# Kernel tuning notes

Hardware: AMD Instinct MI355X
Metric: run time of the kernel (lower is better)

Reference implementation:

```python
import jax, jax.numpy as jnp
import numpy as np
import math

EMBED_DIM = 768
NUM_HEADS = 12
HEAD_DIM = EMBED_DIM // NUM_HEADS
R = 16
LORA_ALPHA = 16
SCALING = LORA_ALPHA / math.sqrt(R)  # 4.0
U = 1.0  # ramp_up_steps=0 -> u()=1.0


def lora_linear(x, W, b, A):
    # base F.linear + SingLoRA delta: delta_W = A @ A.T (symmetric)
    base = x @ W.T + b
    delta_W = A @ A.T  # [D, D]
    return base + (x @ delta_W.T) * (U * SCALING)


def setup_inputs() -> dict:
    key = jax.random.key(0)
    ks = jax.random.split(key, 16)
    B, S, D = 2, 2048, EMBED_DIM
    inv = 1.0 / math.sqrt(D)
    d = {
        'query': jax.random.normal(ks[0], (B, S, D), jnp.float32),
        'key': jax.random.normal(ks[1], (B, S, D), jnp.float32),
        'value': jax.random.normal(ks[2], (B, S, D), jnp.float32),
        'Wq': jax.random.normal(ks[3], (D, D), jnp.float32) * inv,
        'bq': jax.random.normal(ks[4], (D,), jnp.float32) * 0.01,
        'Aq': jax.random.normal(ks[5], (D, R), jnp.float32) * 0.01,
        'Wk': jax.random.normal(ks[6], (D, D), jnp.float32) * inv,
        'bk': jax.random.normal(ks[7], (D,), jnp.float32) * 0.01,
        'Ak': jax.random.normal(ks[8], (D, R), jnp.float32) * 0.01,
        'Wv': jax.random.normal(ks[9], (D, D), jnp.float32) * inv,
        'bv': jax.random.normal(ks[10], (D,), jnp.float32) * 0.01,
        'Av': jax.random.normal(ks[11], (D, R), jnp.float32) * 0.01,
        'Wo': jax.random.normal(ks[12], (D, D), jnp.float32) * inv,
        'bo': jax.random.normal(ks[13], (D,), jnp.float32) * 0.01,
    }
    return d


def reference(query, key, value, Wq, bq, Aq, Wk, bk, Ak, Wv, bv, Av, Wo, bo):
    B, S, D = query.shape
    H, hd = NUM_HEADS, HEAD_DIM
    q = lora_linear(query, Wq, bq, Aq)
    k = lora_linear(key, Wk, bk, Ak)
    v = lora_linear(value, Wv, bv, Av)
    # [B, S, D] -> [B, H, S, hd]
    q = q.reshape(B, S, H, hd).transpose(0, 2, 1, 3)
    k = k.reshape(B, S, H, hd).transpose(0, 2, 1, 3)
    v = v.reshape(B, S, H, hd).transpose(0, 2, 1, 3)
    scores = jnp.einsum('bhqd,bhkd->bhqk', q, k) / math.sqrt(hd)
    attn = jax.nn.softmax(scores, axis=-1)
    out = jnp.einsum('bhqk,bhkd->bhqd', attn, v)  # [B, H, S, hd]
    out = out.transpose(0, 2, 1, 3).reshape(B, S, D)
    out = out @ Wo.T + bo
    return out
```

## Files before the change

### kernel.cpp

```cpp
#include <hip/hip_runtime.h>
#include <math.h>
#include <stdint.h>

#define D 768
#define S 2048
#define B_ 2
#define NROWS 4096
#define H 12
#define HD 64
#define R_ 16

typedef _Float16 half_t;
typedef _Float16 half8 __attribute__((ext_vector_type(8)));
typedef _Float16 half4 __attribute__((ext_vector_type(4)));
typedef float floatx4 __attribute__((ext_vector_type(4)));

#define MFMA32(a, b, c) __builtin_amdgcn_mfma_f32_16x16x32_f16(a, b, c, 0, 0, 0)
#define EXP2F(x) __builtin_amdgcn_exp2f(x)

#define SWAIT(N) __builtin_amdgcn_s_waitcnt(0x0F70 | (N))
#define SBAR() __builtin_amdgcn_s_barrier()
#define SETPRIO(N) __builtin_amdgcn_s_setprio(N)

__device__ __forceinline__ void gl_lds16(const void* gp, half_t* lp) {
  __builtin_amdgcn_global_load_lds(
      (const __attribute__((address_space(1))) void*)(gp),
      (__attribute__((address_space(3))) void*)(lp), 16, 0, 0);
}


__global__ __launch_bounds__(256) void prep_kernel(
    const float* __restrict__ q, const float* __restrict__ k,
    const float* __restrict__ v, half_t* __restrict__ xq,
    half_t* __restrict__ xk, half_t* __restrict__ xv,
    const float* __restrict__ Wq, const float* __restrict__ Aq,
    const float* __restrict__ Wk, const float* __restrict__ Ak,
    const float* __restrict__ Wv, const float* __restrict__ Av,
    const float* __restrict__ Wo, half_t* __restrict__ Mq,
    half_t* __restrict__ Mk, half_t* __restrict__ Mv,
    half_t* __restrict__ Mo) {
  __shared__ float4 As[3072];
  const int bid = blockIdx.x;
  const int tid = threadIdx.x;

  if (bid < 2304) {
    const int y = bid / 768;
    const float* x = (y == 0) ? q : (y == 1) ? k : v;
    half_t* o = (y == 0) ? xq : (y == 1) ? xk : xv;
    const int base = (bid - y * 768) * 4096;
#pragma unroll
    for (int c = 0; c < 4; ++c) {
      int i = base + (tid + 256 * c) * 4;
      float4 vv = *reinterpret_cast<const float4*>(x + i);
      half_t tmp[4] = {(half_t)vv.x, (half_t)vv.y, (half_t)vv.z, (half_t)vv.w};
      *reinterpret_cast<uint64_t*>(o + i) = *reinterpret_cast<uint64_t*>(tmp);
    }
  } else if (bid < 2448) {
    const int base = (bid - 2304) * 4096;
#pragma unroll
    for (int c = 0; c < 4; ++c) {
      int i = base + (tid + 256 * c) * 4;
      float4 vv = *reinterpret_cast<const float4*>(Wo + i);
      half_t tmp[4] = {(half_t)vv.x, (half_t)vv.y, (half_t)vv.z, (half_t)vv.w};
      *reinterpret_cast<uint64_t*>(Mo + i) = *reinterpret_cast<uint64_t*>(tmp);
    }
  } else {
    const int u = bid - 2448;
    const int y = u / 192;
    const int jb = u - y * 192;
    const float* W = (y == 0) ? Wq : (y == 1) ? Wk : Wv;
    const float* A = (y == 0) ? Aq : (y == 1) ? Ak : Av;
    half_t* M = (y == 0) ? Mq : (y == 1) ? Mk : Mv;

#pragma unroll
    for (int c = 0; c < 12; ++c)
      As[tid + 256 * c] =
          *reinterpret_cast<const float4*>(A + (tid + 256 * c) * 4);
    __syncthreads();

    const int j0 = jb * 4;
    float4 aj[4][4];
#pragma unroll
    for (int jj = 0; jj < 4; ++jj)
#pragma unroll
      for (int qq = 0; qq < 4; ++qq) aj[jj][qq] = As[(j0 + jj) * 4 + qq];

#pragma unroll
    for (int c = 0; c < 3; ++c) {
      const int kk = tid + 256 * c;
      float4 ak[4];
#pragma unroll
      for (int qq = 0; qq < 4; ++qq) ak[qq] = As[kk * 4 + qq];
#pragma unroll
      for (int jj = 0; jj < 4; ++jj) {
        float s = 0.f;
#pragma unroll
        for (int qq = 0; qq < 4; ++qq)
          s += ak[qq].x * aj[jj][qq].x + ak[qq].y * aj[jj][qq].y +
               ak[qq].z * aj[jj][qq].z + ak[qq].w * aj[jj][qq].w;
        const int idx = (j0 + jj) * D + kk;
        M[idx] = (half_t)(W[idx] + 4.0f * s);
      }
    }
  }
}

__global__ __launch_bounds__(256) void gemm_qkv_kernel(
    const half_t* __restrict__ x0, const half_t* __restrict__ x1,
    const half_t* __restrict__ x2, const half_t* __restrict__ m0,
    const half_t* __restrict__ m1, const half_t* __restrict__ m2,
    const float* __restrict__ b0, const float* __restrict__ b1,
    const float* __restrict__ b2, half_t* __restrict__ o0,
    half_t* __restrict__ o1, half_t* __restrict__ o2) {
  constexpr int AG = 8;
  constexpr int G = 14;
  constexpr int PB = G * 512;
  __shared__ __align__(16) half_t smem[3 * PB];

  int lin = blockIdx.x + 8 * (blockIdx.y + 32 * blockIdx.z);
  lin = (lin & 7) * 96 + (lin >> 3);
  const int z = lin / 256;
  const int rem = lin - z * 256;
  const int by = rem >> 3;
  const int bx = rem & 7;

  const half_t* X = (z == 0) ? x0 : (z == 1) ? x1 : x2;
  const half_t* M = (z == 0) ? m0 : (z == 1) ? m1 : m2;
  const float* bias = (z == 0) ? b0 : (z == 1) ? b1 : b2;
  half_t* Out = (z == 0) ? o0 : (z == 1) ? o1 : o2;

  const int tid = threadIdx.x;
  const int lane = tid & 63;
  const int wv = tid >> 6;
  const int lr = lane & 15;
  const int lq = lane >> 4;
  const int row0 = by * 128;
  const int j0 = bx * 96;
  const int wr = wv >> 1;
  const int wc = wv & 1;
  const int heavy = __builtin_amdgcn_readfirstlane(wv < 2 ? 1 : 0);

  floatx4 acc[4][3] = {};

#define GSTAGE(soff, k0)                                                      \
  do {                                                                        \
    _Pragma("unroll") for (int gi = 0; gi < 4; ++gi) {                        \
      int g = wv + gi * 4;                                                    \
      if (g < AG) {                                                           \
        gl_lds16(X + (size_t)(row0 + g * 16 + lr) * D + (k0) + lq * 8,        \
                 smem + (soff) + g * 512);                                    \
      } else if (g < G) {                                                     \
        gl_lds16(M + (size_t)(j0 + (g - AG) * 16 + lr) * D + (k0) + lq * 8,   \
                 smem + (soff) + g * 512);                                    \
      }                                                                       \
    }                                                                         \
  } while (0)

#define QWAIT()                                                               \
  do {                                                                        \
    if (heavy) SWAIT(4); else SWAIT(3);                                       \
  } while (0)

  GSTAGE(0, 0);
  GSTAGE(PB, 32);
  QWAIT();
  SBAR();

  int co = 0, so = 2 * PB;
  for (int it = 0; it < D / 32; ++it) {
    if (it + 2 < D / 32) GSTAGE(so, (it + 2) * 32);
    const half_t* Ab = smem + co;
    const half_t* Bb = Ab + AG * 512;
    half8 af[4], bf[3];
#pragma unroll
    for (int t = 0; t < 4; ++t)
      af[t] = *reinterpret_cast<const half8*>(
          &Ab[((wr * 4 + t) * 64 + lane) * 8]);
#pragma unroll
    for (int u = 0; u < 3; ++u)
      bf[u] = *reinterpret_cast<const half8*>(
          &Bb[((wc * 3 + u) * 64 + lane) * 8]);
#pragma unroll
    for (int t = 0; t < 4; ++t)
#pragma unroll
      for (int u = 0; u < 3; ++u) acc[t][u] = MFMA32(af[t], bf[u], acc[t][u]);
    if (it + 2 < D / 32) QWAIT(); else SWAIT(0);
    SBAR();
    co += PB; if (co == 3 * PB) co = 0;
    so += PB; if (so == 3 * PB) so = 0;
  }
#undef GSTAGE
#undef QWAIT

  float bv[3];
#pragma unroll
  for (int u = 0; u < 3; ++u) bv[u] = bias[j0 + (wc * 3 + u) * 16 + lr];

  if (z == 2) {
    const int bb = row0 >> 11;
    const int kb0 = (row0 & 2047) >> 6;
#pragma unroll
    for (int t = 0; t < 4; ++t) {
#pragma unroll
      for (int u = 0; u < 3; ++u) {
        int gc = j0 + (wc * 3 + u) * 16 + lr;
        int hh = gc >> 6;
        int ud = (gc & 63) >> 4;
        half4 hv;
#pragma unroll
        for (int r = 0; r < 4; ++r) hv[r] = (half_t)(acc[t][u][r] + bv[u]);
        size_t addr = ((size_t)(bb * H + hh) * HD) * S +
                      (size_t)(kb0 + wr) * 4096 +
                      (ud * 2 + ((t >> 1) & 1)) * 512 + lane * 8 + (t & 1) * 4;
        *reinterpret_cast<half4*>(&Out[addr]) = hv;
      }
    }
    return;
  }

#pragma unroll
  for (int t = 0; t < 4; ++t) {
#pragma unroll
    for (int u = 0; u < 3; ++u) {
#pragma unroll
      for (int r = 0; r < 4; ++r) {
        int gr = row0 + (wr * 4 + t) * 16 + lq * 4 + r;
        int gc = j0 + (wc * 3 + u) * 16 + lr;
        Out[(size_t)gr * D + gc] = (half_t)(acc[t][u][r] + bv[u]);
      }
    }
  }
}

__global__ __launch_bounds__(256) void gemm_o_kernel(
    const half_t* __restrict__ Xh, const half_t* __restrict__ M,
    const float* __restrict__ bias, float* __restrict__ Out) {
  constexpr int AG = 8;
  constexpr int G = 16;
  constexpr int PB = G * 512;
  __shared__ __align__(16) half_t smem[3 * PB];

  int lin = blockIdx.x + 12 * blockIdx.y;
  lin = (lin & 7) * 96 + (lin >> 3);
  const int bx = lin % 12;
  const int byy = lin / 12;

  const int tid = threadIdx.x;
  const int lane = tid & 63;
  const int wv = tid >> 6;
  const int lr = lane & 15;
  const int lq = lane >> 4;
  const int row0 = byy * 64;
  const int j0 = bx * 64;
  const int wr = wv >> 1;
  const int wc = wv & 1;

  floatx4 acc[2][2] = {};

#define GSTAGE(soff, k0)                                                       \
  do {                                                                         \
    _Pragma("unroll") for (int gi = 0; gi < 4; ++gi) {                         \
      int g = wv * 4 + gi;                                                     \
      if (g < AG) {                                                            \
        int t = g >> 1, c = g & 1;                                             \
        gl_lds16(                                                              \
            Xh + (size_t)(row0 + t * 16 + lr) * D + (k0) + c * 32 + lq * 8,    \
            smem + (soff) + g * 512);                                          \
      } else {                                                                 \
        int g2 = g - AG;                                                       \
        int u = g2 >> 1, c = g2 & 1;                                           \
        gl_lds16(                                                              \
            M + (size_t)(j0 + u * 16 + lr) * D + (k0) + c * 32 + lq * 8,       \
            smem + (soff) + AG * 512 + g2 * 512);                              \
      }                                                                        \
    }                                                                          \
  } while (0)

  GSTAGE(0, 0);
  GSTAGE(PB, 64);
  SWAIT(4);
  SBAR();

  int co = 0, so = 2 * PB;
  for (int it = 0; it < D / 64; ++it) {
    if (it + 2 < D / 64) GSTAGE(so, (it + 2) * 64);
    const half_t* Ab = smem + co;
    const half_t* Bb = Ab + AG * 512;
#pragma unroll
    for (int c = 0; c < 2; ++c) {
      half8 af[2], bf[2];
#pragma unroll
      for (int t = 0; t < 2; ++t)
        af[t] = *reinterpret_cast<const half8*>(
            &Ab[(((wr * 2 + t) * 2 + c) * 64 + lane) * 8]);
#pragma unroll
      for (int u = 0; u < 2; ++u)
        bf[u] = *reinterpret_cast<const half8*>(
            &Bb[(((wc * 2 + u) * 2 + c) * 64 + lane) * 8]);
#pragma unroll
      for (int t = 0; t < 2; ++t)
#pragma unroll
        for (int u = 0; u < 2; ++u) acc[t][u] = MFMA32(af[t], bf[u], acc[t][u]);
    }
    if (it + 2 < D / 64) SWAIT(4); else SWAIT(0);
    SBAR();
    co += PB; if (co == 3 * PB) co = 0;
    so += PB; if (so == 3 * PB) so = 0;
  }
#undef GSTAGE

  float bv[2];
#pragma unroll
  for (int u = 0; u < 2; ++u) bv[u] = bias[j0 + (wc * 2 + u) * 16 + lr];
#pragma unroll
  for (int t = 0; t < 2; ++t) {
#pragma unroll
    for (int u = 0; u < 2; ++u) {
#pragma unroll
      for (int r = 0; r < 4; ++r) {
        int gr = row0 + (wr * 2 + t) * 16 + lq * 4 + r;
        int gc = j0 + (wc * 2 + u) * 16 + lr;
        Out[(size_t)gr * D + gc] = acc[t][u][r] + bv[u];
      }
    }
  }
}

__global__ __launch_bounds__(256, 3) void attn_mfma_kernel(
    const half_t* __restrict__ Qh, const half_t* __restrict__ Kh,
    const half_t* __restrict__ Vt2, half_t* __restrict__ Oh) {
  __shared__ __align__(16) half_t smem[24576];
  half_t* Ks = smem;
  half_t* Vs = smem + 12288;

  const int tid = threadIdx.x;
  const int lane = tid & 63;
  const int wv = tid >> 6;
  const int qp = wv >> 1;
  const int half_ = wv & 1;
  const int lr = lane & 15;
  const int lq = lane >> 4;

  int lin = blockIdx.x + 32 * (blockIdx.y + 12 * blockIdx.z);
  lin = (lin & 7) * 96 + (lin >> 3);
  const int q0 = (lin & 31) * 64;
  const int hb = lin >> 5;
  const int h = hb % 12;
  const int b = hb / 12;

  const size_t base = (size_t)b * S * D + h * HD;
  const size_t vtbase = (size_t)(b * H + h) * HD * (size_t)S;

  const half_t qscale = (half_t)0.18033688f;
  half8 qf[2][2];
#pragma unroll
  for (int s = 0; s < 2; ++s) {
    const int qw = q0 + (qp * 2 + s) * 16;
#pragma unroll
    for (int c = 0; c < 2; ++c) {
      half8 qv = *reinterpret_cast<const half8*>(
          &Qh[base + (size_t)(qw + lr) * D + c * 32 + lq * 8]);
#pragma unroll
      for (int j = 0; j < 8; ++j) qv[j] = qv[j] * qscale;
      qf[s][c] = qv;
    }
  }

  half8 ones8;
#pragma unroll
  for (int j = 0; j < 8; ++j) ones8[j] = (half_t)1.0f;

  floatx4 o[2][4] = {};
  floatx4 ol[2] = {};

#define STAGE(soff, kb)                                                        \
  do {                                                                         \
    _Pragma("unroll") for (int gi = 0; gi < 4; ++gi) {                         \
      int g = wv * 4 + gi;                                                     \
      if (g < 8) {                                                             \
        int u = g >> 1, c = g & 1;                                             \
        gl_lds16(                                                              \
            Kh + base + (size_t)((kb) + u * 16 + lr) * D + c * 32 + lq * 8,    \
            Ks + (soff) + g * 512);                                            \
      } else {                                                                 \
        int gv = g - 8;                                                        \
        gl_lds16(Vt2 + vtbase + (size_t)(kb)*64 + gv * 512 + lane * 8,         \
                 Vs + (soff) + gv * 512);                                      \
      }                                                                        \
    }                                                                          \
  } while (0)

  STAGE(0, 0);
  STAGE(4096, 64);
  SWAIT(4);
  SBAR();

  int co = 0, so = 8192;
  for (int it = 0; it < S / 64; ++it) {
    if (it + 2 < S / 64) STAGE(so, (it + 2) * 64);

    half8 pv[2];
#pragma unroll
    for (int ui = 0; ui < 2; ++ui) {
      const int u = half_ * 2 + ui;
      half8 kf0 = *reinterpret_cast<const half8*>(
          &Ks[co + ((u * 2 + 0) * 64 + lane) * 8]);
      half8 kf1 = *reinterpret_cast<const half8*>(
          &Ks[co + ((u * 2 + 1) * 64 + lane) * 8]);
      SETPRIO(1);
      floatx4 st0 = {}, st1 = {};
      st0 = MFMA32(kf0, qf[0][0], st0);
      st0 = MFMA32(kf1, qf[0][1], st0);
      st1 = MFMA32(kf0, qf[1][0], st1);
      st1 = MFMA32(kf1, qf[1][1], st1);
      SETPRIO(0);
#pragma unroll
      for (int j = 0; j < 4; ++j) {
        pv[0][4 * ui + j] = (half_t)EXP2F(st0[j]);
        pv[1][4 * ui + j] = (half_t)EXP2F(st1[j]);
      }
    }
    SETPRIO(1);
#pragma unroll
    for (int ud = 0; ud < 4; ++ud) {
      half8 vf8 = *reinterpret_cast<const half8*>(
          &Vs[co + ((ud * 2 + half_) * 64 + lane) * 8]);
      o[0][ud] = MFMA32(pv[0], vf8, o[0][ud]);
      o[1][ud] = MFMA32(pv[1], vf8, o[1][ud]);
    }
    ol[0] = MFMA32(pv[0], ones8, ol[0]);
    ol[1] = MFMA32(pv[1], ones8, ol[1]);
    SETPRIO(0);

    if (it + 2 < S / 64) SWAIT(4); else SWAIT(0);
    SBAR();
    co += 4096; if (co == 12288) co = 0;
    so += 4096; if (so == 12288) so = 0;
  }
#undef STAGE

  float* red = (float*)smem;
  if (half_ == 1) {
#pragma unroll
    for (int s = 0; s < 2; ++s) {
      const int slot = (qp * 2 + s) * 64 + lane;
#pragma unroll
      for (int comp = 0; comp < 16; ++comp)
        red[comp * 260 + slot] = o[s][comp >> 2][comp & 3];
#pragma unroll
      for (int r = 0; r < 4; ++r) red[(16 + r) * 260 + slot] = ol[s][r];
    }
  }
  __syncthreads();
  if (half_ == 0) {
#pragma unroll
    for (int s = 0; s < 2; ++s) {
      const int slot = (qp * 2 + s) * 64 + lane;
      const int qw = q0 + (qp * 2 + s) * 16;
      float linv[4];
#pragma unroll
      for (int r = 0; r < 4; ++r)
        linv[r] = 1.0f / (ol[s][r] + red[(16 + r) * 260 + slot]);
#pragma unroll
      for (int ud = 0; ud < 4; ++ud) {
#pragma unroll
        for (int r = 0; r < 4; ++r) {
          float ov = o[s][ud][r] + red[(ud * 4 + r) * 260 + slot];
          int row = qw + lq * 4 + r;
          int col = h * HD + ud * 16 + lr;
          Oh[(size_t)(b * S + row) * D + col] = (half_t)(ov * linv[r]);
        }
      }
    }
  }
}

extern "C" void kernel_launch(void* const* d_in, const int* in_sizes, int n_in,
                              void* d_out, int out_size, void* d_ws,
                              size_t ws_size, hipStream_t stream) {
  const float* query = (const float*)d_in[0];
  const float* key   = (const float*)d_in[1];
  const float* value = (const float*)d_in[2];
  const float* Wq = (const float*)d_in[3];
  const float* bq = (const float*)d_in[4];
  const float* Aq = (const float*)d_in[5];
  const float* Wk = (const float*)d_in[6];
  const float* bk = (const float*)d_in[7];
  const float* Ak = (const float*)d_in[8];
  const float* Wv = (const float*)d_in[9];
  const float* bv = (const float*)d_in[10];
  const float* Av = (const float*)d_in[11];
  const float* Wo = (const float*)d_in[12];
  const float* bo = (const float*)d_in[13];
  float* out = (float*)d_out;

  half_t* hw = (half_t*)d_ws;
  const size_t XSZ = (size_t)NROWS * D;
  const size_t MSZ = (size_t)D * D;
  half_t* xq = hw;
  half_t* xk = xq + XSZ;
  half_t* xv = xk + XSZ;
  half_t* qh = xv + XSZ;
  half_t* kh = qh + XSZ;
  half_t* vt = kh + XSZ;
  half_t* ab = vt + XSZ;
  half_t* Mq = ab + XSZ;
  half_t* Mk = Mq + MSZ;
  half_t* Mv = Mk + MSZ;
  half_t* Mo = Mv + MSZ;

  prep_kernel<<<3024, 256, 0, stream>>>(query, key, value, xq, xk, xv, Wq, Aq,
                                        Wk, Ak, Wv, Av, Wo, Mq, Mk, Mv, Mo);

  dim3 gq(D / 96, NROWS / 128, 3);
  gemm_qkv_kernel<<<gq, 256, 0, stream>>>(xq, xk, xv, Mq, Mk, Mv, bq, bk, bv,
                                          qh, kh, vt);

  dim3 ga(S / 64, H, B_);
  attn_mfma_kernel<<<ga, 256, 0, stream>>>(qh, kh, vt, ab);

  dim3 go(D / 64, NROWS / 64, 1);
  gemm_o_kernel<<<go, 256, 0, stream>>>(ab, Mo, bo, out);
}
```

Before: 200.8 us.

## Give each wave private double-buffered LDS slices to remove per-tile block barriers

Each wave now stages only the K and V chunks it consumes into its own private LDS region, double-buffered. This removes the shared triple-buffered staging and the per-iteration block-wide barrier. Synchronization becomes per-wave vmcnt and lgkmcnt waits, and the LDS footprint grows to 64KB, so launch bounds drop from 3 to 2 blocks per SU. The trade-off is lower occupancy and duplicated loads of K across the two waves of each pair in exchange for barrier-free pipelining.

```diff
diff --git a/kernel.cpp b/kernel.cpp
--- a/kernel.cpp
+++ b/kernel.cpp
@@ -19,6 +19,7 @@
 #define EXP2F(x) __builtin_amdgcn_exp2f(x)
 
 #define SWAIT(N) __builtin_amdgcn_s_waitcnt(0x0F70 | (N))
+#define LGWAIT() __builtin_amdgcn_s_waitcnt(0xC07F)
 #define SBAR() __builtin_amdgcn_s_barrier()
 #define SETPRIO(N) __builtin_amdgcn_s_setprio(N)
 
@@ -326,12 +327,10 @@
   }
 }
 
-__global__ __launch_bounds__(256, 3) void attn_mfma_kernel(
+__global__ __launch_bounds__(256, 2) void attn_mfma_kernel(
     const half_t* __restrict__ Qh, const half_t* __restrict__ Kh,
     const half_t* __restrict__ Vt2, half_t* __restrict__ Oh) {
-  __shared__ __align__(16) half_t smem[24576];
-  half_t* Ks = smem;
-  half_t* Vs = smem + 12288;
+  __shared__ __align__(16) half_t smem[32768];
 
   const int tid = threadIdx.x;
   const int lane = tid & 63;
@@ -351,6 +350,8 @@
   const size_t base = (size_t)b * S * D + h * HD;
   const size_t vtbase = (size_t)(b * H + h) * HD * (size_t)S;
 
+  half_t* W0 = smem + wv * 8192;
+
   const half_t qscale = (half_t)0.18033688f;
   half8 qf[2][2];
 #pragma unroll
@@ -373,72 +374,69 @@
   floatx4 o[2][4] = {};
   floatx4 ol[2] = {};
 
-#define STAGE(soff, kb)                                                        \
+#define STAGE(so_, kb)                                                         \
   do {                                                                         \
-    _Pragma("unroll") for (int gi = 0; gi < 4; ++gi) {                         \
-      int g = wv * 4 + gi;                                                     \
-      if (g < 8) {                                                             \
-        int u = g >> 1, c = g & 1;                                             \
-        gl_lds16(                                                              \
-            Kh + base + (size_t)((kb) + u * 16 + lr) * D + c * 32 + lq * 8,    \
-            Ks + (soff) + g * 512);                                            \
-      } else {                                                                 \
-        int gv = g - 8;                                                        \
-        gl_lds16(Vt2 + vtbase + (size_t)(kb)*64 + gv * 512 + lane * 8,         \
-                 Vs + (soff) + gv * 512);                                      \
+    _Pragma("unroll") for (int ui = 0; ui < 2; ++ui)                           \
+      _Pragma("unroll") for (int c = 0; c < 2; ++c)                            \
+        gl_lds16(Kh + base +                                                   \
+                     (size_t)((kb) + (half_ * 2 + ui) * 16 + lr) * D +         \
+                     c * 32 + lq * 8,                                          \
+                 W0 + (so_) + (ui * 2 + c) * 512);                             \
+    _Pragma("unroll") for (int ud = 0; ud < 4; ++ud)                           \
+      gl_lds16(Vt2 + vtbase + (size_t)(kb) * 64 + (ud * 2 + half_) * 512 +     \
+                   lane * 8,                                                   \
+               W0 + (so_) + 2048 + ud * 512);                                  \
+  } while (0)
+
+#define COMP(so_)                                                              \
+  do {                                                                         \
+    half8 pv[2];                                                               \
+    _Pragma("unroll") for (int ui = 0; ui < 2; ++ui) {                         \
+      half8 kf0 = *reinterpret_cast<const half8*>(                             \
+          &W0[(so_) + (ui * 2 + 0) * 512 + lane * 8]);                         \
+      half8 kf1 = *reinterpret_cast<const half8*>(                             \
+          &W0[(so_) + (ui * 2 + 1) * 512 + lane * 8]);                         \
+      SETPRIO(1);                                                              \
+      floatx4 st0 = {}, st1 = {};                                              \
+      st0 = MFMA32(kf0, qf[0][0], st0);                                        \
+      st0 = MFMA32(kf1, qf[0][1], st0);                                        \
+      st1 = MFMA32(kf0, qf[1][0], st1);                                        \
+      st1 = MFMA32(kf1, qf[1][1], st1);                                        \
+      SETPRIO(0);                                                              \
+      _Pragma("unroll") for (int j = 0; j < 4; ++j) {                          \
+        pv[0][4 * ui + j] = (half_t)EXP2F(st0[j]);                             \
+        pv[1][4 * ui + j] = (half_t)EXP2F(st1[j]);                             \
       }                                                                        \
     }                                                                          \
+    SETPRIO(1);                                                                \
+    _Pragma("unroll") for (int ud = 0; ud < 4; ++ud) {                         \
+      half8 vf8 = *reinterpret_cast<const half8*>(                             \
+          &W0[(so_) + 2048 + ud * 512 + lane * 8]);                            \
+      o[0][ud] = MFMA32(pv[0], vf8, o[0][ud]);                                 \
+      o[1][ud] = MFMA32(pv[1], vf8, o[1][ud]);                                 \
+    }                                                                          \
+    ol[0] = MFMA32(pv[0], ones8, ol[0]);                                       \
+    ol[1] = MFMA32(pv[1], ones8, ol[1]);                                       \
+    SETPRIO(0);                                                                \
   } while (0)
 
   STAGE(0, 0);
   STAGE(4096, 64);
-  SWAIT(4);
-  SBAR();
-
-  int co = 0, so = 8192;
-  for (int it = 0; it < S / 64; ++it) {
-    if (it + 2 < S / 64) STAGE(so, (it + 2) * 64);
-
-    half8 pv[2];
-#pragma unroll
-    for (int ui = 0; ui < 2; ++ui) {
-      const int u = half_ * 2 + ui;
-      half8 kf0 = *reinterpret_cast<const half8*>(
-          &Ks[co + ((u * 2 + 0) * 64 + lane) * 8]);
-      half8 kf1 = *reinterpret_cast<const half8*>(
-          &Ks[co + ((u * 2 + 1) * 64 + lane) * 8]);
-      SETPRIO(1);
-      floatx4 st0 = {}, st1 = {};
-      st0 = MFMA32(kf0, qf[0][0], st0);
-      st0 = MFMA32(kf1, qf[0][1], st0);
-      st1 = MFMA32(kf0, qf[1][0], st1);
-      st1 = MFMA32(kf1, qf[1][1], st1);
-      SETPRIO(0);
-#pragma unroll
-      for (int j = 0; j < 4; ++j) {
-        pv[0][4 * ui + j] = (half_t)EXP2F(st0[j]);
-        pv[1][4 * ui + j] = (half_t)EXP2F(st1[j]);
-      }
-    }
-    SETPRIO(1);
-#pragma unroll
-    for (int ud = 0; ud < 4; ++ud) {
-      half8 vf8 = *reinterpret_cast<const half8*>(
-          &Vs[co + ((ud * 2 + half_) * 64 + lane) * 8]);
-      o[0][ud] = MFMA32(pv[0], vf8, o[0][ud]);
-      o[1][ud] = MFMA32(pv[1], vf8, o[1][ud]);
-    }
-    ol[0] = MFMA32(pv[0], ones8, ol[0]);
-    ol[1] = MFMA32(pv[1], ones8, ol[1]);
-    SETPRIO(0);
-
-    if (it + 2 < S / 64) SWAIT(4); else SWAIT(0);
-    SBAR();
-    co += 4096; if (co == 12288) co = 0;
-    so += 4096; if (so == 12288) so = 0;
+
+  int so = 0;
+  for (int it = 0; it < 32; ++it) {
+    if (it < 31) SWAIT(8); else SWAIT(0);
+    COMP(so);
+    if (it + 2 < 32) {
+      LGWAIT();
+      STAGE(so, (it + 2) * 64);
+    }
+    so ^= 4096;
   }
 #undef STAGE
-
+#undef COMP
+
+  __syncthreads();
   float* red = (float*)smem;
   if (half_ == 1) {
 #pragma unroll
```

New measurement: 223.2 us. 1.11x slower.
